# Performance work log

Measured on AMD Instinct MI355X. Metric: run time of the kernel, lower is better.

The kernel has to match this reference:

```python
import jax, jax.numpy as jnp
import numpy as np


def setup_inputs() -> dict:
    key = jax.random.key(0)
    kq, kk, kv = jax.random.split(key, 3)
    B, S, D = 8, 4096, 64
    q = jax.random.normal(kq, (B, S, D), dtype=jnp.float32)
    k = jax.random.normal(kk, (B, S, D), dtype=jnp.float32)
    v = jax.random.normal(kv, (B, S, D), dtype=jnp.float32)
    mask = jnp.ones((B, S), dtype=jnp.float32)
    return {"q": q, "k": k, "v": v, "mask": mask}


def reference(q, k, v, mask):
    # scores: [B, Sq, Sk], scaled by sqrt(D)
    scale = 1.0 / jnp.sqrt(jnp.asarray(q.shape[-1], q.dtype))
    w = jnp.einsum("bqd,bkd->bqk", q, k) * scale
    # softmax over dim=2 (keys axis for rank-3 input)
    w = jax.nn.softmax(w, axis=2)
    x = jnp.einsum("bqk,bkd->bqd", w, v)
    # post-hoc multiplicative mask on outputs
    x = x * mask[..., None]
    return x
```

## Files before the change

### kernel.cpp

```cpp
#include <hip/hip_runtime.h>

typedef __attribute__((ext_vector_type(8))) short short8;
typedef __attribute__((ext_vector_type(4))) float floatx4;
typedef __attribute__((ext_vector_type(4))) unsigned short ushortx4;
typedef __attribute__((ext_vector_type(8))) unsigned short ushortx8;
typedef unsigned int u32;
typedef __attribute__((ext_vector_type(2))) u32 u32x2;
typedef __attribute__((ext_vector_type(4))) u32 u32x4;

#define MFMA_K32(A, B, C) __builtin_amdgcn_mfma_f32_16x16x32_bf16(A, B, C, 0, 0, 0)

#if __has_builtin(__builtin_amdgcn_exp2f)
#define EXP2(x) __builtin_amdgcn_exp2f(x)
#else
#define EXP2(x) exp2f(x)
#endif

#define WAIT_VM12() __builtin_amdgcn_s_waitcnt(0x0F7C)
#define WAIT_VM8() __builtin_amdgcn_s_waitcnt(0x0F78)
#define WAIT_VM0() __builtin_amdgcn_s_waitcnt(0x0F70)
#define SB0() __builtin_amdgcn_sched_barrier(0)

__device__ __forceinline__ unsigned short f2bf(float f) {
  u32 u = __builtin_bit_cast(u32, f);
  u += 0x7FFFu + ((u >> 16) & 1u);
  return (unsigned short)(u >> 16);
}
__device__ __forceinline__ void load_lds16(const void* g, void* l) {
  __builtin_amdgcn_global_load_lds((const __attribute__((address_space(1))) u32*)g,
                                   (__attribute__((address_space(3))) u32*)l, 16, 0, 0);
}

__global__ __launch_bounds__(256) void prep_kv(
    const float* __restrict__ k, const float* __restrict__ v,
    unsigned short* __restrict__ kb, unsigned short* __restrict__ vt) {
  __shared__ float tileT[64 * 68];
  const int blk = blockIdx.x, tid = threadIdx.x;
  size_t base = (size_t)blk * 4096 + tid * 4;
#pragma unroll
  for (int i = 0; i < 4; i++) {
    size_t off = base + (size_t)i * 1024;
    floatx4 f = *(const floatx4*)(k + off);
    ushortx4 h;
    h[0] = f2bf(f[0]); h[1] = f2bf(f[1]); h[2] = f2bf(f[2]); h[3] = f2bf(f[3]);
    *(ushortx4*)(kb + off) = h;
  }
  const int b = blk >> 6, h = blk & 63;
  const int r = tid >> 2, c4 = (tid & 3) * 16;
  const float* vp = v + ((size_t)b * 4096 + h * 64 + r) * 64 + c4;
#pragma unroll
  for (int i = 0; i < 4; i++) {
    floatx4 f = *(const floatx4*)(vp + i * 4);
#pragma unroll
    for (int j = 0; j < 4; j++) tileT[(c4 + i * 4 + j) * 68 + r] = f[j];
  }
  __syncthreads();
  const int d = tid >> 2, g = tid & 3;
  unsigned short* vb = vt + (size_t)b * 262144 + ((h >> 1) * 4 + (h & 1) * 2) * 2048;
#pragma unroll
  for (int s = 0; s < 2; s++) {
    const float* src = tileT + d * 68 + s * 32 + g * 8;
    floatx4 f0 = *(const floatx4*)src;
    floatx4 f1 = *(const floatx4*)(src + 4);
    ushortx8 hh;
#pragma unroll
    for (int j = 0; j < 4; j++) { hh[j] = f2bf(f0[j]); hh[4 + j] = f2bf(f1[j]); }
    *(ushortx8*)(vb + s * 2048 + d * 32 + g * 8) = hh;
  }
}

__global__ __launch_bounds__(256, 2) void attn(
    const float* __restrict__ q, const unsigned short* __restrict__ kb,
    const unsigned short* __restrict__ vt, const float* __restrict__ mask,
    float* __restrict__ out) {
  __shared__ __align__(16) char smem_raw[65536];
  unsigned short* smem = (unsigned short*)smem_raw;
  const int tid = threadIdx.x;
  const int wave = tid >> 6, lane = tid & 63;
  const int c = lane & 15, quad = lane >> 4;
  const int b = blockIdx.x & 7, qt = blockIdx.x >> 3;
  const int q0 = qt * 64;

  const unsigned short* kB = kb + (size_t)b * (4096 * 64);
  const unsigned short* vtB = vt + (size_t)b * 262144;

  const float qscale = 0.18033688011112042f;
  short8 qf[4][2];
#pragma unroll
  for (int nt = 0; nt < 4; nt++)
#pragma unroll
    for (int kc = 0; kc < 2; kc++) {
      const float* qp = q + ((size_t)b * 4096 + q0 + nt * 16 + c) * 64 + kc * 32 + quad * 8;
      floatx4 f0 = *(const floatx4*)qp;
      floatx4 f1 = *(const floatx4*)(qp + 4);
      short8 s;
#pragma unroll
      for (int j = 0; j < 4; j++) {
        s[j] = (short)f2bf(f0[j] * qscale);
        s[4 + j] = (short)f2bf(f1[j] * qscale);
      }
      qf[nt][kc] = s;
    }

  floatx4 o[4][4], o_l[4];
#pragma unroll
  for (int mt = 0; mt < 4; mt++)
#pragma unroll
    for (int nt = 0; nt < 4; nt++) o[mt][nt] = (floatx4){0.f, 0.f, 0.f, 0.f};
#pragma unroll
  for (int nt = 0; nt < 4; nt++) o_l[nt] = (floatx4){0.f, 0.f, 0.f, 0.f};

  short8 ones8;
#pragma unroll
  for (int j = 0; j < 8; j++) ones8[j] = (short)0x3F80;

  const int r8 = lane >> 3, cs8 = lane & 7;
  const int klane = (r8 >> 2) * 8 + (r8 & 3);
  unsigned short* wbase = smem + wave * 8192;
  const unsigned short* gK0 = kB + (size_t)(wave * 32 + klane) * 64 + (cs8 ^ r8) * 8;
  const unsigned short* gV0 = vtB + wave * 2048 + c * 32 + quad * 8;

  auto stageK = [&](int t, int buf) {
    unsigned short* Kd = wbase + buf * 2048;
    const unsigned short* gk = gK0 + (size_t)t * 8192;
    load_lds16(gk, Kd);
    load_lds16(gk + 16 * 64, Kd + 512);
    load_lds16(gk + 4 * 64, Kd + 1024);
    load_lds16(gk + 20 * 64, Kd + 1536);
  };
  auto loadV = [&](u32x4* vv, int t) {
    const unsigned short* gv = gV0 + (size_t)t * 8192;
#pragma unroll
    for (int mt = 0; mt < 4; mt++) vv[mt] = *(const u32x4*)(gv + mt * 512);
  };

  auto compute = [&](const unsigned short* Kbuf, const u32x4* vv) {
    short8 kfA[2], kfB[2];
#pragma unroll
    for (int kc = 0; kc < 2; kc++) {
      const int sl = ((kc * 4 + quad) ^ (c & 7)) * 8;
      kfA[kc] = *(const short8*)(Kbuf + c * 64 + sl);
      kfB[kc] = *(const short8*)(Kbuf + 1024 + c * 64 + sl);
    }
#pragma unroll
    for (int nt = 0; nt < 4; nt++) {
      floatx4 sA = (floatx4){0.f, 0.f, 0.f, 0.f}, sB = sA;
      sA = MFMA_K32(kfA[0], qf[nt][0], sA);
      sA = MFMA_K32(kfA[1], qf[nt][1], sA);
      sB = MFMA_K32(kfB[0], qf[nt][0], sB);
      sB = MFMA_K32(kfB[1], qf[nt][1], sB);
      u32 a0 = __builtin_bit_cast(u32, EXP2(sA[0]));
      u32 a1 = __builtin_bit_cast(u32, EXP2(sA[1]));
      u32 a2 = __builtin_bit_cast(u32, EXP2(sA[2]));
      u32 a3 = __builtin_bit_cast(u32, EXP2(sA[3]));
      u32 b0 = __builtin_bit_cast(u32, EXP2(sB[0]));
      u32 b1 = __builtin_bit_cast(u32, EXP2(sB[1]));
      u32 b2 = __builtin_bit_cast(u32, EXP2(sB[2]));
      u32 b3 = __builtin_bit_cast(u32, EXP2(sB[3]));
      u32x4 pw = {__builtin_amdgcn_perm(a1, a0, 0x07060302u),
                  __builtin_amdgcn_perm(a3, a2, 0x07060302u),
                  __builtin_amdgcn_perm(b1, b0, 0x07060302u),
                  __builtin_amdgcn_perm(b3, b2, 0x07060302u)};
      short8 pf = __builtin_bit_cast(short8, pw);
#pragma unroll
      for (int mt = 0; mt < 4; mt++)
        o[mt][nt] = MFMA_K32(__builtin_bit_cast(short8, vv[mt]), pf, o[mt][nt]);
      o_l[nt] = MFMA_K32(ones8, pf, o_l[nt]);
    }
  };

  u32x4 vvA[4], vvB[4];
  stageK(0, 0);
  loadV(vvA, 0);
  stageK(1, 1);

#pragma unroll 1
  for (int tt = 0; tt < 16; tt++) {
    const int t0 = 2 * tt, t1 = t0 + 1;
    loadV(vvB, t1);
    if (t0 + 2 < 32) { stageK(t0 + 2, (t0 + 2) & 3); WAIT_VM12(); }
    else { WAIT_VM8(); }
    SB0();
    compute(wbase + (t0 & 3) * 2048, vvA);
    if (t1 + 2 < 32) { loadV(vvA, t1 + 1); stageK(t1 + 2, (t1 + 2) & 3); WAIT_VM12(); }
    else { WAIT_VM0(); }
    SB0();
    compute(wbase + (t1 & 3) * 2048, vvB);
  }

  __syncthreads();
  float* obuf = (float*)smem_raw;
  float* lbuf = obuf + 9216;
  if (lane < 16) {
#pragma unroll
    for (int nt = 0; nt < 4; nt++) lbuf[wave * 64 + nt * 16 + c] = o_l[nt][0];
  }
  if (wave < 2) {
    float* ob = obuf + wave * 4608;
#pragma unroll
    for (int mt = 0; mt < 4; mt++)
#pragma unroll
      for (int nt = 0; nt < 4; nt++)
        *(floatx4*)(ob + (nt * 16 + c) * 72 + mt * 16 + quad * 4) = o[mt][nt];
  }
  __syncthreads();
  if (wave >= 2) {
    float* ob = obuf + (wave - 2) * 4608;
#pragma unroll
    for (int mt = 0; mt < 4; mt++)
#pragma unroll
      for (int nt = 0; nt < 4; nt++) {
        float* a = ob + (nt * 16 + c) * 72 + mt * 16 + quad * 4;
        floatx4 cur = *(floatx4*)a;
        *(floatx4*)a = cur + o[mt][nt];
      }
  }
  __syncthreads();

  const int row = tid >> 2, dg = (tid & 3) * 16;
  const float l = lbuf[row] + lbuf[64 + row] + lbuf[128 + row] + lbuf[192 + row];
  const float sc = mask[b * 4096 + q0 + row] / l;
  float* op = out + ((size_t)b * 4096 + q0 + row) * 64 + dg;
#pragma unroll
  for (int i = 0; i < 4; i++) {
    floatx4 a = *(const floatx4*)(obuf + row * 72 + dg + i * 4);
    floatx4 b2 = *(const floatx4*)(obuf + 4608 + row * 72 + dg + i * 4);
    *(floatx4*)(op + i * 4) = (a + b2) * sc;
  }
}

extern "C" void kernel_launch(void* const* d_in, const int* in_sizes, int n_in,
                              void* d_out, int out_size, void* d_ws, size_t ws_size,
                              hipStream_t stream) {
  const float* q = (const float*)d_in[0];
  const float* k = (const float*)d_in[1];
  const float* v = (const float*)d_in[2];
  const float* mask = (const float*)d_in[3];
  unsigned short* kb = (unsigned short*)d_ws;
  unsigned short* vt = kb + 8 * 4096 * 64;
  prep_kv<<<512, 256, 0, stream>>>(k, v, kb, vt);
  attn<<<512, 256, 0, stream>>>(q, kb, vt, mask, (float*)d_out);
}
```

Baseline: 117.2 us.

## Split key range across eight waves per block with double-buffered K staging

Each block now launches 512 threads, so eight waves split the 4096 keys and each wave processes 16 tiles instead of 32. K staging in LDS drops from four buffers to two per wave, with stricter waits that overlap less load with compute. The final reduction now merges eight per-wave partial outputs in three serialized LDS rounds. The extra per-block parallelism shortens each block's sequential loop, at the cost of a longer reduction and less load/compute overlap.

Result: slower. 383.7 us (+227.5%).

```diff
diff --git a/kernel.cpp b/kernel.cpp
--- a/kernel.cpp
+++ b/kernel.cpp
@@ -16,7 +16,6 @@
 #define EXP2(x) exp2f(x)
 #endif
 
-#define WAIT_VM12() __builtin_amdgcn_s_waitcnt(0x0F7C)
 #define WAIT_VM8() __builtin_amdgcn_s_waitcnt(0x0F78)
 #define WAIT_VM0() __builtin_amdgcn_s_waitcnt(0x0F70)
 #define SB0() __builtin_amdgcn_sched_barrier(0)
@@ -69,7 +68,7 @@
   }
 }
 
-__global__ __launch_bounds__(256, 2) void attn(
+__global__ __launch_bounds__(512, 4) void attn(
     const float* __restrict__ q, const unsigned short* __restrict__ kb,
     const unsigned short* __restrict__ vt, const float* __restrict__ mask,
     float* __restrict__ out) {
@@ -116,20 +115,20 @@
 
   const int r8 = lane >> 3, cs8 = lane & 7;
   const int klane = (r8 >> 2) * 8 + (r8 & 3);
-  unsigned short* wbase = smem + wave * 8192;
+  unsigned short* wbase = smem + wave * 4096;
   const unsigned short* gK0 = kB + (size_t)(wave * 32 + klane) * 64 + (cs8 ^ r8) * 8;
   const unsigned short* gV0 = vtB + wave * 2048 + c * 32 + quad * 8;
 
   auto stageK = [&](int t, int buf) {
     unsigned short* Kd = wbase + buf * 2048;
-    const unsigned short* gk = gK0 + (size_t)t * 8192;
+    const unsigned short* gk = gK0 + (size_t)t * 16384;
     load_lds16(gk, Kd);
     load_lds16(gk + 16 * 64, Kd + 512);
     load_lds16(gk + 4 * 64, Kd + 1024);
     load_lds16(gk + 20 * 64, Kd + 1536);
   };
   auto loadV = [&](u32x4* vv, int t) {
-    const unsigned short* gv = gV0 + (size_t)t * 8192;
+    const unsigned short* gv = gV0 + (size_t)t * 16384;
 #pragma unroll
     for (int mt = 0; mt < 4; mt++) vv[mt] = *(const u32x4*)(gv + mt * 512);
   };
@@ -175,18 +174,28 @@
   stageK(1, 1);
 
 #pragma unroll 1
-  for (int tt = 0; tt < 16; tt++) {
-    const int t0 = 2 * tt, t1 = t0 + 1;
-    loadV(vvB, t1);
-    if (t0 + 2 < 32) { stageK(t0 + 2, (t0 + 2) & 3); WAIT_VM12(); }
-    else { WAIT_VM8(); }
-    SB0();
-    compute(wbase + (t0 & 3) * 2048, vvA);
-    if (t1 + 2 < 32) { loadV(vvA, t1 + 1); stageK(t1 + 2, (t1 + 2) & 3); WAIT_VM12(); }
-    else { WAIT_VM0(); }
-    SB0();
-    compute(wbase + (t1 & 3) * 2048, vvB);
-  }
+  for (int tt = 0; tt < 7; tt++) {
+    const int t0 = 2 * tt;
+    loadV(vvB, t0 + 1);
+    WAIT_VM8();
+    SB0();
+    compute(wbase, vvA);
+    SB0();
+    stageK(t0 + 2, 0);
+    loadV(vvA, t0 + 2);
+    WAIT_VM8();
+    SB0();
+    compute(wbase + 2048, vvB);
+    SB0();
+    stageK(t0 + 3, 1);
+  }
+  loadV(vvB, 15);
+  WAIT_VM8();
+  SB0();
+  compute(wbase, vvA);
+  WAIT_VM0();
+  SB0();
+  compute(wbase + 2048, vvB);
 
   __syncthreads();
   float* obuf = (float*)smem_raw;
@@ -204,25 +213,30 @@
         *(floatx4*)(ob + (nt * 16 + c) * 72 + mt * 16 + quad * 4) = o[mt][nt];
   }
   __syncthreads();
-  if (wave >= 2) {
-    float* ob = obuf + (wave - 2) * 4608;
-#pragma unroll
-    for (int mt = 0; mt < 4; mt++)
-#pragma unroll
-      for (int nt = 0; nt < 4; nt++) {
-        float* a = ob + (nt * 16 + c) * 72 + mt * 16 + quad * 4;
-        floatx4 cur = *(floatx4*)a;
-        *(floatx4*)a = cur + o[mt][nt];
-      }
-  }
-  __syncthreads();
-
-  const int row = tid >> 2, dg = (tid & 3) * 16;
-  const float l = lbuf[row] + lbuf[64 + row] + lbuf[128 + row] + lbuf[192 + row];
+#pragma unroll 1
+  for (int rr = 1; rr < 4; rr++) {
+    if (wave == 2 * rr || wave == 2 * rr + 1) {
+      float* ob = obuf + (wave - 2 * rr) * 4608;
+#pragma unroll
+      for (int mt = 0; mt < 4; mt++)
+#pragma unroll
+        for (int nt = 0; nt < 4; nt++) {
+          float* a = ob + (nt * 16 + c) * 72 + mt * 16 + quad * 4;
+          floatx4 cur = *(floatx4*)a;
+          *(floatx4*)a = cur + o[mt][nt];
+        }
+    }
+    __syncthreads();
+  }
+
+  const int row = tid >> 3, dg = (tid & 7) * 8;
+  float l = 0.f;
+#pragma unroll
+  for (int w = 0; w < 8; w++) l += lbuf[w * 64 + row];
   const float sc = mask[b * 4096 + q0 + row] / l;
   float* op = out + ((size_t)b * 4096 + q0 + row) * 64 + dg;
 #pragma unroll
-  for (int i = 0; i < 4; i++) {
+  for (int i = 0; i < 2; i++) {
     floatx4 a = *(const floatx4*)(obuf + row * 72 + dg + i * 4);
     floatx4 b2 = *(const floatx4*)(obuf + 4608 + row * 72 + dg + i * 4);
     *(floatx4*)(op + i * 4) = (a + b2) * sc;
@@ -239,5 +253,5 @@
   unsigned short* kb = (unsigned short*)d_ws;
   unsigned short* vt = kb + 8 * 4096 * 64;
   prep_kv<<<512, 256, 0, stream>>>(k, v, kb, vt);
-  attn<<<512, 256, 0, stream>>>(q, kb, vt, mask, (float*)d_out);
-}
+  attn<<<512, 512, 0, stream>>>(q, kb, vt, mask, (float*)d_out);
+}
```

## Software-pipeline K fragment LDS reads ahead of compute and add MFMA priority hints

Applied to the files above, without the earlier changes.

Restructures the main loop so the K fragments for the next tile are read from LDS into registers before the current tile's compute, unrolling by four with fixed buffer indices. The aim is to hide LDS read latency behind MFMA work. It also wraps the MFMA groups in s_setprio raises and drops the min-blocks hint from launch bounds. In exchange it holds more live registers, which could reduce occupancy or cause spills. The wait counts also change to match the new issue order.

New measurement: 129.8 us. 10.8% more time.

```diff
diff --git a/kernel.cpp b/kernel.cpp
--- a/kernel.cpp
+++ b/kernel.cpp
@@ -16,8 +16,8 @@
 #define EXP2(x) exp2f(x)
 #endif
 
-#define WAIT_VM12() __builtin_amdgcn_s_waitcnt(0x0F7C)
 #define WAIT_VM8() __builtin_amdgcn_s_waitcnt(0x0F78)
+#define WAIT_VM4() __builtin_amdgcn_s_waitcnt(0x0F74)
 #define WAIT_VM0() __builtin_amdgcn_s_waitcnt(0x0F70)
 #define SB0() __builtin_amdgcn_sched_barrier(0)
 
@@ -69,7 +69,7 @@
   }
 }
 
-__global__ __launch_bounds__(256, 2) void attn(
+__global__ __launch_bounds__(256) void attn(
     const float* __restrict__ q, const unsigned short* __restrict__ kb,
     const unsigned short* __restrict__ vt, const float* __restrict__ mask,
     float* __restrict__ out) {
@@ -134,21 +134,26 @@
     for (int mt = 0; mt < 4; mt++) vv[mt] = *(const u32x4*)(gv + mt * 512);
   };
 
-  auto compute = [&](const unsigned short* Kbuf, const u32x4* vv) {
-    short8 kfA[2], kfB[2];
+  struct KF { short8 A[2]; short8 B[2]; };
+  auto readKF = [&](const unsigned short* Kbuf, KF& kf) {
 #pragma unroll
     for (int kc = 0; kc < 2; kc++) {
       const int sl = ((kc * 4 + quad) ^ (c & 7)) * 8;
-      kfA[kc] = *(const short8*)(Kbuf + c * 64 + sl);
-      kfB[kc] = *(const short8*)(Kbuf + 1024 + c * 64 + sl);
+      kf.A[kc] = *(const short8*)(Kbuf + c * 64 + sl);
+      kf.B[kc] = *(const short8*)(Kbuf + 1024 + c * 64 + sl);
     }
+  };
+
+  auto compute = [&](const KF& kf, const u32x4* vv) {
 #pragma unroll
     for (int nt = 0; nt < 4; nt++) {
       floatx4 sA = (floatx4){0.f, 0.f, 0.f, 0.f}, sB = sA;
-      sA = MFMA_K32(kfA[0], qf[nt][0], sA);
-      sA = MFMA_K32(kfA[1], qf[nt][1], sA);
-      sB = MFMA_K32(kfB[0], qf[nt][0], sB);
-      sB = MFMA_K32(kfB[1], qf[nt][1], sB);
+      __builtin_amdgcn_s_setprio(1);
+      sA = MFMA_K32(kf.A[0], qf[nt][0], sA);
+      sA = MFMA_K32(kf.A[1], qf[nt][1], sA);
+      sB = MFMA_K32(kf.B[0], qf[nt][0], sB);
+      sB = MFMA_K32(kf.B[1], qf[nt][1], sB);
+      __builtin_amdgcn_s_setprio(0);
       u32 a0 = __builtin_bit_cast(u32, EXP2(sA[0]));
       u32 a1 = __builtin_bit_cast(u32, EXP2(sA[1]));
       u32 a2 = __builtin_bit_cast(u32, EXP2(sA[2]));
@@ -162,31 +167,60 @@
                   __builtin_amdgcn_perm(b1, b0, 0x07060302u),
                   __builtin_amdgcn_perm(b3, b2, 0x07060302u)};
       short8 pf = __builtin_bit_cast(short8, pw);
+      __builtin_amdgcn_s_setprio(1);
 #pragma unroll
       for (int mt = 0; mt < 4; mt++)
         o[mt][nt] = MFMA_K32(__builtin_bit_cast(short8, vv[mt]), pf, o[mt][nt]);
       o_l[nt] = MFMA_K32(ones8, pf, o_l[nt]);
+      __builtin_amdgcn_s_setprio(0);
     }
   };
 
   u32x4 vvA[4], vvB[4];
+  KF kfE, kfO;
   stageK(0, 0);
   loadV(vvA, 0);
   stageK(1, 1);
+  WAIT_VM8(); SB0();
+  readKF(wbase, kfE);
 
 #pragma unroll 1
-  for (int tt = 0; tt < 16; tt++) {
-    const int t0 = 2 * tt, t1 = t0 + 1;
-    loadV(vvB, t1);
-    if (t0 + 2 < 32) { stageK(t0 + 2, (t0 + 2) & 3); WAIT_VM12(); }
-    else { WAIT_VM8(); }
-    SB0();
-    compute(wbase + (t0 & 3) * 2048, vvA);
-    if (t1 + 2 < 32) { loadV(vvA, t1 + 1); stageK(t1 + 2, (t1 + 2) & 3); WAIT_VM12(); }
-    else { WAIT_VM0(); }
-    SB0();
-    compute(wbase + (t1 & 3) * 2048, vvB);
-  }
+  for (int it = 0; it < 7; it++) {
+    const int t0 = 4 * it;
+    loadV(vvB, t0 + 1); stageK(t0 + 2, 2);
+    WAIT_VM8(); SB0();
+    readKF(wbase + 2048, kfO);
+    compute(kfE, vvA); SB0();
+
+    loadV(vvA, t0 + 2); stageK(t0 + 3, 3);
+    WAIT_VM8(); SB0();
+    readKF(wbase + 4096, kfE);
+    compute(kfO, vvB); SB0();
+
+    loadV(vvB, t0 + 3); stageK(t0 + 4, 0);
+    WAIT_VM8(); SB0();
+    readKF(wbase + 6144, kfO);
+    compute(kfE, vvA); SB0();
+
+    loadV(vvA, t0 + 4); stageK(t0 + 5, 1);
+    WAIT_VM8(); SB0();
+    readKF(wbase, kfE);
+    compute(kfO, vvB); SB0();
+  }
+  loadV(vvB, 29); stageK(30, 2);
+  WAIT_VM8(); SB0();
+  readKF(wbase + 2048, kfO);
+  compute(kfE, vvA); SB0();
+  loadV(vvA, 30); stageK(31, 3);
+  WAIT_VM8(); SB0();
+  readKF(wbase + 4096, kfE);
+  compute(kfO, vvB); SB0();
+  loadV(vvB, 31);
+  WAIT_VM4(); SB0();
+  readKF(wbase + 6144, kfO);
+  compute(kfE, vvA); SB0();
+  WAIT_VM0(); SB0();
+  compute(kfO, vvB);
 
   __syncthreads();
   float* obuf = (float*)smem_raw;
```

## Split attention key range across two blocks and add finalize reduction kernel

Applied to the files above, without the earlier changes.

Splits the key dimension into two halves, launching 1024 blocks instead of 512 so the GPU's compute units are better filled, then adds a finalize kernel that sums the partial outputs and row sums and applies mask and normalization. It also replaces the ones-vector MFMA used for the softmax denominator with a scalar accumulation plus cross-lane shuffles, and shrinks the K LDS ring from four buffers to three to allow more resident blocks. Costs are an extra kernel launch and a global round-trip for the partial outputs. Since there is no running max, summing the two halves stays exact.

Measured after the change: 151.6 us. 29.4% more time.

```diff
diff --git a/kernel.cpp b/kernel.cpp
--- a/kernel.cpp
+++ b/kernel.cpp
@@ -5,7 +5,6 @@
 typedef __attribute__((ext_vector_type(4))) unsigned short ushortx4;
 typedef __attribute__((ext_vector_type(8))) unsigned short ushortx8;
 typedef unsigned int u32;
-typedef __attribute__((ext_vector_type(2))) u32 u32x2;
 typedef __attribute__((ext_vector_type(4))) u32 u32x4;
 
 #define MFMA_K32(A, B, C) __builtin_amdgcn_mfma_f32_16x16x32_bf16(A, B, C, 0, 0, 0)
@@ -69,16 +68,20 @@
   }
 }
 
-__global__ __launch_bounds__(256, 2) void attn(
+template <int NSPLIT>
+__global__ __launch_bounds__(256) void attn(
     const float* __restrict__ q, const unsigned short* __restrict__ kb,
     const unsigned short* __restrict__ vt, const float* __restrict__ mask,
-    float* __restrict__ out) {
-  __shared__ __align__(16) char smem_raw[65536];
+    float* __restrict__ out, float* __restrict__ pbuf, float* __restrict__ lws) {
+  constexpr int NT = 32 / NSPLIT;
+  __shared__ __align__(16) char smem_raw[49152];
   unsigned short* smem = (unsigned short*)smem_raw;
   const int tid = threadIdx.x;
   const int wave = tid >> 6, lane = tid & 63;
   const int c = lane & 15, quad = lane >> 4;
-  const int b = blockIdx.x & 7, qt = blockIdx.x >> 3;
+  const int blk = blockIdx.x & 511;
+  const int kh = blockIdx.x >> 9;
+  const int b = blk & 7, qt = blk >> 3;
   const int q0 = qt * 64;
 
   const unsigned short* kB = kb + (size_t)b * (4096 * 64);
@@ -102,39 +105,38 @@
       qf[nt][kc] = s;
     }
 
-  floatx4 o[4][4], o_l[4];
+  floatx4 o[4][4];
+  float l_acc[4];
 #pragma unroll
   for (int mt = 0; mt < 4; mt++)
 #pragma unroll
     for (int nt = 0; nt < 4; nt++) o[mt][nt] = (floatx4){0.f, 0.f, 0.f, 0.f};
 #pragma unroll
-  for (int nt = 0; nt < 4; nt++) o_l[nt] = (floatx4){0.f, 0.f, 0.f, 0.f};
-
-  short8 ones8;
-#pragma unroll
-  for (int j = 0; j < 8; j++) ones8[j] = (short)0x3F80;
+  for (int nt = 0; nt < 4; nt++) l_acc[nt] = 0.f;
 
   const int r8 = lane >> 3, cs8 = lane & 7;
   const int klane = (r8 >> 2) * 8 + (r8 & 3);
-  unsigned short* wbase = smem + wave * 8192;
-  const unsigned short* gK0 = kB + (size_t)(wave * 32 + klane) * 64 + (cs8 ^ r8) * 8;
-  const unsigned short* gV0 = vtB + wave * 2048 + c * 32 + quad * 8;
-
-  auto stageK = [&](int t, int buf) {
-    unsigned short* Kd = wbase + buf * 2048;
-    const unsigned short* gk = gK0 + (size_t)t * 8192;
-    load_lds16(gk, Kd);
-    load_lds16(gk + 16 * 64, Kd + 512);
-    load_lds16(gk + 4 * 64, Kd + 1024);
-    load_lds16(gk + 20 * 64, Kd + 1536);
+  unsigned short* wbase = smem + wave * 6144;
+  const unsigned short* kstage = kB + (size_t)(kh * NT) * 8192 +
+                                 (size_t)(wave * 32 + klane) * 64 + (cs8 ^ r8) * 8;
+  const unsigned short* vload = vtB + (size_t)(kh * NT) * 8192 + wave * 2048 + c * 32 + quad * 8;
+
+  auto stageK = [&](u32 off) {
+    unsigned short* Kd = wbase + off;
+    load_lds16(kstage, Kd);
+    load_lds16(kstage + 16 * 64, Kd + 512);
+    load_lds16(kstage + 4 * 64, Kd + 1024);
+    load_lds16(kstage + 20 * 64, Kd + 1536);
+    kstage += 8192;
   };
-  auto loadV = [&](u32x4* vv, int t) {
-    const unsigned short* gv = gV0 + (size_t)t * 8192;
-#pragma unroll
-    for (int mt = 0; mt < 4; mt++) vv[mt] = *(const u32x4*)(gv + mt * 512);
+  auto loadV = [&](u32x4* vv) {
+#pragma unroll
+    for (int mt = 0; mt < 4; mt++) vv[mt] = *(const u32x4*)(vload + mt * 512);
+    vload += 8192;
   };
 
-  auto compute = [&](const unsigned short* Kbuf, const u32x4* vv) {
+  auto compute = [&](u32 off, const u32x4* vv) {
+    const unsigned short* Kbuf = wbase + off;
     short8 kfA[2], kfB[2];
 #pragma unroll
     for (int kc = 0; kc < 2; kc++) {
@@ -149,14 +151,13 @@
       sA = MFMA_K32(kfA[1], qf[nt][1], sA);
       sB = MFMA_K32(kfB[0], qf[nt][0], sB);
       sB = MFMA_K32(kfB[1], qf[nt][1], sB);
-      u32 a0 = __builtin_bit_cast(u32, EXP2(sA[0]));
-      u32 a1 = __builtin_bit_cast(u32, EXP2(sA[1]));
-      u32 a2 = __builtin_bit_cast(u32, EXP2(sA[2]));
-      u32 a3 = __builtin_bit_cast(u32, EXP2(sA[3]));
-      u32 b0 = __builtin_bit_cast(u32, EXP2(sB[0]));
-      u32 b1 = __builtin_bit_cast(u32, EXP2(sB[1]));
-      u32 b2 = __builtin_bit_cast(u32, EXP2(sB[2]));
-      u32 b3 = __builtin_bit_cast(u32, EXP2(sB[3]));
+      float eA0 = EXP2(sA[0]), eA1 = EXP2(sA[1]), eA2 = EXP2(sA[2]), eA3 = EXP2(sA[3]);
+      float eB0 = EXP2(sB[0]), eB1 = EXP2(sB[1]), eB2 = EXP2(sB[2]), eB3 = EXP2(sB[3]);
+      l_acc[nt] += ((eA0 + eA1) + (eA2 + eA3)) + ((eB0 + eB1) + (eB2 + eB3));
+      u32 a0 = __builtin_bit_cast(u32, eA0), a1 = __builtin_bit_cast(u32, eA1);
+      u32 a2 = __builtin_bit_cast(u32, eA2), a3 = __builtin_bit_cast(u32, eA3);
+      u32 b0 = __builtin_bit_cast(u32, eB0), b1 = __builtin_bit_cast(u32, eB1);
+      u32 b2 = __builtin_bit_cast(u32, eB2), b3 = __builtin_bit_cast(u32, eB3);
       u32x4 pw = {__builtin_amdgcn_perm(a1, a0, 0x07060302u),
                   __builtin_amdgcn_perm(a3, a2, 0x07060302u),
                   __builtin_amdgcn_perm(b1, b0, 0x07060302u),
@@ -165,27 +166,41 @@
 #pragma unroll
       for (int mt = 0; mt < 4; mt++)
         o[mt][nt] = MFMA_K32(__builtin_bit_cast(short8, vv[mt]), pf, o[mt][nt]);
-      o_l[nt] = MFMA_K32(ones8, pf, o_l[nt]);
     }
   };
 
   u32x4 vvA[4], vvB[4];
-  stageK(0, 0);
-  loadV(vvA, 0);
-  stageK(1, 1);
-
+  stageK(0);
+  loadV(vvA);
+  stageK(2048);
+  u32 bo = 0;
 #pragma unroll 1
-  for (int tt = 0; tt < 16; tt++) {
-    const int t0 = 2 * tt, t1 = t0 + 1;
-    loadV(vvB, t1);
-    if (t0 + 2 < 32) { stageK(t0 + 2, (t0 + 2) & 3); WAIT_VM12(); }
-    else { WAIT_VM8(); }
-    SB0();
-    compute(wbase + (t0 & 3) * 2048, vvA);
-    if (t1 + 2 < 32) { loadV(vvA, t1 + 1); stageK(t1 + 2, (t1 + 2) & 3); WAIT_VM12(); }
-    else { WAIT_VM0(); }
-    SB0();
-    compute(wbase + (t1 & 3) * 2048, vvB);
+  for (int it = 0; it < (NT - 2) / 2; ++it) {
+    u32 s1 = bo + 4096; if (s1 >= 6144) s1 -= 6144;
+    loadV(vvB); stageK(s1);
+    WAIT_VM12(); SB0();
+    compute(bo, vvA); SB0();
+
+    u32 b1 = bo + 2048; if (b1 >= 6144) b1 -= 6144;
+    loadV(vvA); stageK(bo);
+    WAIT_VM12(); SB0();
+    compute(b1, vvB); SB0();
+    bo = s1;
+  }
+  loadV(vvB);
+  WAIT_VM8(); SB0();
+  compute(bo, vvA); SB0();
+  WAIT_VM0(); SB0();
+  u32 bl = bo + 2048; if (bl >= 6144) bl -= 6144;
+  compute(bl, vvB);
+
+  float lw[4];
+#pragma unroll
+  for (int nt = 0; nt < 4; nt++) {
+    float l = l_acc[nt];
+    l += __shfl_xor(l, 16);
+    l += __shfl_xor(l, 32);
+    lw[nt] = l;
   }
 
   __syncthreads();
@@ -193,7 +208,7 @@
   float* lbuf = obuf + 9216;
   if (lane < 16) {
 #pragma unroll
-    for (int nt = 0; nt < 4; nt++) lbuf[wave * 64 + nt * 16 + c] = o_l[nt][0];
+    for (int nt = 0; nt < 4; nt++) lbuf[wave * 64 + nt * 16 + c] = lw[nt];
   }
   if (wave < 2) {
     float* ob = obuf + wave * 4608;
@@ -218,15 +233,43 @@
   __syncthreads();
 
   const int row = tid >> 2, dg = (tid & 3) * 16;
-  const float l = lbuf[row] + lbuf[64 + row] + lbuf[128 + row] + lbuf[192 + row];
-  const float sc = mask[b * 4096 + q0 + row] / l;
-  float* op = out + ((size_t)b * 4096 + q0 + row) * 64 + dg;
-#pragma unroll
-  for (int i = 0; i < 4; i++) {
-    floatx4 a = *(const floatx4*)(obuf + row * 72 + dg + i * 4);
-    floatx4 b2 = *(const floatx4*)(obuf + 4608 + row * 72 + dg + i * 4);
-    *(floatx4*)(op + i * 4) = (a + b2) * sc;
-  }
+  const float lsum = lbuf[row] + lbuf[64 + row] + lbuf[128 + row] + lbuf[192 + row];
+  if constexpr (NSPLIT == 1) {
+    const float sc = mask[b * 4096 + q0 + row] / lsum;
+    float* op = out + ((size_t)b * 4096 + q0 + row) * 64 + dg;
+#pragma unroll
+    for (int i = 0; i < 4; i++) {
+      floatx4 a = *(const floatx4*)(obuf + row * 72 + dg + i * 4);
+      floatx4 b2 = *(const floatx4*)(obuf + 4608 + row * 72 + dg + i * 4);
+      *(floatx4*)(op + i * 4) = (a + b2) * sc;
+    }
+  } else {
+    float* dst = (kh ? (pbuf + (size_t)blk * 4096)
+                     : (out + ((size_t)b * 4096 + q0) * 64)) + row * 64 + dg;
+#pragma unroll
+    for (int i = 0; i < 4; i++) {
+      floatx4 a = *(const floatx4*)(obuf + row * 72 + dg + i * 4);
+      floatx4 b2 = *(const floatx4*)(obuf + 4608 + row * 72 + dg + i * 4);
+      *(floatx4*)(dst + i * 4) = a + b2;
+    }
+    if ((tid & 3) == 0) lws[blk * 128 + kh * 64 + row] = lsum;
+  }
+}
+
+__global__ __launch_bounds__(256) void finalize(
+    const float* __restrict__ mask, const float* __restrict__ pbuf,
+    const float* __restrict__ lws, float* __restrict__ out) {
+  const int blk = blockIdx.x;
+  const int b = blk & 7, qt = blk >> 3;
+  const int row = threadIdx.x >> 2, dg = (threadIdx.x & 3) * 16;
+  const float l = lws[blk * 128 + row] + lws[blk * 128 + 64 + row];
+  const float sc = mask[b * 4096 + qt * 64 + row] / l;
+  float* op = out + ((size_t)b * 4096 + qt * 64 + row) * 64 + dg;
+  const float* pp = pbuf + (size_t)blk * 4096 + row * 64 + dg;
+#pragma unroll
+  for (int i = 0; i < 4; i++)
+    *(floatx4*)(op + i * 4) =
+        (*(const floatx4*)(op + i * 4) + *(const floatx4*)(pp + i * 4)) * sc;
 }
 
 extern "C" void kernel_launch(void* const* d_in, const int* in_sizes, int n_in,
@@ -238,6 +281,16 @@
   const float* mask = (const float*)d_in[3];
   unsigned short* kb = (unsigned short*)d_ws;
   unsigned short* vt = kb + 8 * 4096 * 64;
+  const size_t base = (size_t)8 * 1024 * 1024;
+  const size_t need = base + (size_t)512 * 4096 * 4 + (size_t)512 * 128 * 4;
   prep_kv<<<512, 256, 0, stream>>>(k, v, kb, vt);
-  attn<<<512, 256, 0, stream>>>(q, kb, vt, mask, (float*)d_out);
-}
+  if (ws_size >= need) {
+    float* pbuf = (float*)((char*)d_ws + base);
+    float* lws = pbuf + (size_t)512 * 4096;
+    attn<2><<<1024, 256, 0, stream>>>(q, kb, vt, mask, (float*)d_out, pbuf, lws);
+    finalize<<<512, 256, 0, stream>>>(mask, pbuf, lws, (float*)d_out);
+  } else {
+    attn<1><<<512, 256, 0, stream>>>(q, kb, vt, mask, (float*)d_out,
+                                     (float*)d_out, (float*)d_out);
+  }
+}
```
